# Kernel optimization log

Measured on AMD Instinct MI355X. Metric: run time of the kernel, lower is better.

Reference implementation:

```python
import jax, jax.numpy as jnp
import numpy as np

B, T, D, H, J = 64, 128, 768, 256, 128  # batch, tokens, input_dim, span_hidden_dim, top_injection_dim
PRUNING_RATIO = 2.0


def setup_inputs() -> dict:
    key = jax.random.key(0)
    ks = jax.random.split(key, 12)
    def w(k, shape, fan_in):
        return jax.random.normal(k, shape, jnp.float32) / np.sqrt(fan_in)
    return {
        "inputs": jax.random.normal(ks[0], (B, T, D), jnp.float32),
        "input_mask": jnp.ones((B, T), jnp.int32),
        "top_injection_embedding": jax.random.normal(ks[1], (B, J), jnp.float32),
        # SpanRepAssembly: start / end projections
        "W_start": w(ks[2], (D, H), D), "b_start": jnp.zeros((H,), jnp.float32),
        "W_end": w(ks[3], (D, H), D), "b_end": jnp.zeros((H,), jnp.float32),
        # span_scorer: ReLU -> Linear(H,H) -> ReLU -> Linear(H,1)
        "W_s1": w(ks[4], (H, H), H), "b_s1": jnp.zeros((H,), jnp.float32),
        "W_s2": w(ks[5], (H, 1), H), "b_s2": jnp.zeros((1,), jnp.float32),
        # top injection path
        "W_inj": w(ks[6], (J, H), J), "b_inj": jnp.zeros((H,), jnp.float32),
        "W_sec": w(ks[7], (H, H), H), "b_sec": jnp.zeros((H,), jnp.float32),
        "W_pred": w(ks[8], (H, 1), H), "b_pred": jnp.zeros((1,), jnp.float32),
    }


def reference(inputs, input_mask, top_injection_embedding,
              W_start, b_start, W_end, b_end,
              W_s1, b_s1, W_s2, b_s2,
              W_inj, b_inj, W_sec, b_sec, W_pred, b_pred):
    b, t, _ = inputs.shape
    k_spans = int(PRUNING_RATIO * t)
    # SpanRepAssembly: span_hidden[b, (s,e)] = startProj(x_s) + endProj(x_e), s <= e,
    # flattened start-major (matches start_end_range ordering).
    A = inputs @ W_start + b_start                      # [B,T,H]
    E = inputs @ W_end + b_end                          # [B,T,H]
    s_idx, e_idx = jnp.triu_indices(t)                  # N = T(T+1)/2 spans, row-major
    span_hidden = A[:, s_idx] + E[:, e_idx]             # [B,N,H]
    m = input_mask.astype(jnp.float32)
    span_mask = m[:, s_idx] * m[:, e_idx]               # [B,N]
    # span_scorer MLP over all spans
    h = jax.nn.relu(span_hidden) @ W_s1 + b_s1
    scores = (jax.nn.relu(h) @ W_s2 + b_s2)[..., 0]     # [B,N]
    # SpanPruner: mask invalid spans to -inf, top-k, sort indices, gather
    masked_scores = jnp.where(span_mask > 0, scores, -jnp.inf)
    _, top_idx = jax.lax.top_k(masked_scores, k_spans)  # [B,K]
    top_idx = jnp.sort(top_idx, axis=1)
    top_span_hidden = jnp.take_along_axis(span_hidden, top_idx[:, :, None], axis=1)  # [B,K,H]
    top_span_mask = jnp.take_along_axis(span_mask, top_idx, axis=1)[..., None]       # [B,K,1]
    top_span_scores = jnp.take_along_axis(masked_scores, top_idx, axis=1)[..., None] # [B,K,1]
    top_span_scores = jnp.where(jnp.isinf(top_span_scores), -1.0, top_span_scores)
    # top-injection scoring head
    inj = (top_injection_embedding @ W_inj + b_inj)[:, None, :]      # [B,1,H]
    sec = top_span_hidden @ W_sec + b_sec                            # [B,K,H]
    top_span_logits = jax.nn.relu(inj + sec) @ W_pred + b_pred + top_span_scores  # [B,K,1]
    top_span_probs = jax.nn.sigmoid(top_span_logits) * top_span_mask
    return top_span_probs
```

## Files before the change

kernel.cpp:

```cpp
#include <hip/hip_runtime.h>
#include <hip/hip_bf16.h>
#include <math.h>

#define BB 64
#define T 128
#define DD 768
#define H 256
#define JJ 128
#define NSPAN 8256
#define KTOP 256
#define SCAP 1024
#define MARGIN 0.03f

typedef __attribute__((ext_vector_type(8))) short bf16x8;
typedef __attribute__((ext_vector_type(4))) float f32x4;

__device__ inline unsigned short bfrne(float x) {
    unsigned u = __float_as_uint(x);
    return (unsigned short)((u + 0x7FFFu + ((u >> 16) & 1u)) >> 16);
}

__device__ inline unsigned pk2(float x, float y) {
    float2 f; f.x = x; f.y = y;
    __hip_bfloat162 h = __float22bfloat162_rn(f);
    return *reinterpret_cast<unsigned*>(&h);
}

template<int CTRL>
__device__ __forceinline__ float dpp_add16(float v) {
    return v + __int_as_float(__builtin_amdgcn_update_dpp(
        0, __float_as_int(v), CTRL, 0xF, 0xF, true));
}

__global__ __launch_bounds__(256) void prep_proj_kernel(
    const float* __restrict__ X,
    const float* __restrict__ Wa, const float* __restrict__ ba,
    const float* __restrict__ Wb, const float* __restrict__ bb,
    float* __restrict__ AE,
    int* __restrict__ s_idx, int* __restrict__ e_idx,
    const float* __restrict__ W1, unsigned short* __restrict__ Wpk,
    const float* __restrict__ tie, const float* __restrict__ Winj,
    const float* __restrict__ binj, float* __restrict__ injv)
{
    const int blk = blockIdx.x;
    const int t = threadIdx.x;

    if (blk >= 512) {
        const int pblk = blk - 512;
        if (pblk == 0) {
            if (t < T) {
                int s = t;
                int start = s * T - (s * (s - 1)) / 2;
                int len = T - s;
                for (int i = 0; i < len; ++i) {
                    s_idx[start + i] = s;
                    e_idx[start + i] = s + i;
                }
            }
        } else if (pblk <= 256) {
            int idx = (pblk - 1) * 256 + t;
            int j  = idx & 7;
            int l  = (idx >> 3) & 63;
            int kc = (idx >> 9) & 7;
            int ct = idx >> 12;
            int k = kc * 32 + (l >> 4) * 8 + j;
            int n = ct * 16 + (l & 15);
            Wpk[idx] = bfrne(W1[k * 256 + n]);
        } else {
            int b = pblk - 257;
            __shared__ float tb[JJ];
            if (t < JJ) tb[t] = tie[b * JJ + t];
            __syncthreads();
            float a = binj[t];
            for (int j = 0; j < JJ; ++j)
                a = fmaf(tb[j], Winj[j * H + t], a);
            injv[b * H + t] = a;
        }
        return;
    }

    const int px = blk & 127;
    const int cb = blk >> 7;
    const int m0 = px * 64;
    const float* W    = (cb < 2) ? Wa : Wb;
    const float* bias = (cb < 2) ? ba : bb;
    const int wc0 = (cb & 1) * 128;
    const int oc0 = (cb < 2) ? wc0 : (256 + wc0);

    __shared__ float Xs[64 * 36];
    __shared__ float Wl[32 * 132];

    const int tx = t & 15;
    const int ty = t >> 4;

    const int xrow = t >> 2;
    const int xk8  = (t & 3) * 8;
    const int wrow = t >> 4;
    const int wcol = (t & 15) * 8;

    float4 xr[2], w0r[2], w1r[2];
    {
        const float* xp = &X[(size_t)(m0 + xrow) * DD + xk8];
        xr[0] = *(const float4*)&xp[0]; xr[1] = *(const float4*)&xp[4];
        const float* wp0 = &W[(size_t)wrow * 256 + wc0 + wcol];
        w0r[0] = *(const float4*)&wp0[0]; w0r[1] = *(const float4*)&wp0[4];
        const float* wp1 = &W[(size_t)(wrow + 16) * 256 + wc0 + wcol];
        w1r[0] = *(const float4*)&wp1[0]; w1r[1] = *(const float4*)&wp1[4];
    }

    float acc[4][8];
#pragma unroll
    for (int i = 0; i < 4; ++i)
#pragma unroll
        for (int j = 0; j < 8; ++j) acc[i][j] = 0.f;

    for (int it = 0; it < 24; ++it) {
        __syncthreads();
        *(float4*)&Xs[xrow * 36 + xk8]           = xr[0];
        *(float4*)&Xs[xrow * 36 + xk8 + 4]       = xr[1];
        *(float4*)&Wl[wrow * 132 + wcol]         = w0r[0];
        *(float4*)&Wl[wrow * 132 + wcol + 4]     = w0r[1];
        *(float4*)&Wl[(wrow+16) * 132 + wcol]    = w1r[0];
        *(float4*)&Wl[(wrow+16) * 132 + wcol + 4]= w1r[1];
        __syncthreads();
        if (it + 1 < 24) {
            const int kk = (it + 1) * 32;
            const float* xp = &X[(size_t)(m0 + xrow) * DD + kk + xk8];
            xr[0] = *(const float4*)&xp[0]; xr[1] = *(const float4*)&xp[4];
            const float* wp0 = &W[(size_t)(kk + wrow) * 256 + wc0 + wcol];
            w0r[0] = *(const float4*)&wp0[0]; w0r[1] = *(const float4*)&wp0[4];
            const float* wp1 = &W[(size_t)(kk + wrow + 16) * 256 + wc0 + wcol];
            w1r[0] = *(const float4*)&wp1[0]; w1r[1] = *(const float4*)&wp1[4];
        }
#pragma unroll
        for (int k = 0; k < 32; ++k) {
            float4 wv0 = *(const float4*)&Wl[k * 132 + tx * 8];
            float4 wv1 = *(const float4*)&Wl[k * 132 + tx * 8 + 4];
            float wq[8] = {wv0.x, wv0.y, wv0.z, wv0.w, wv1.x, wv1.y, wv1.z, wv1.w};
            float xq[4];
#pragma unroll
            for (int i = 0; i < 4; ++i)
                xq[i] = Xs[(ty * 4 + i) * 36 + k];
#pragma unroll
            for (int i = 0; i < 4; ++i)
#pragma unroll
                for (int j = 0; j < 8; ++j)
                    acc[i][j] = fmaf(xq[i], wq[j], acc[i][j]);
        }
    }

    float bq[8];
#pragma unroll
    for (int j = 0; j < 8; ++j) bq[j] = bias[wc0 + tx * 8 + j];
#pragma unroll
    for (int i = 0; i < 4; ++i) {
        const size_t row = m0 + ty * 4 + i;
        float4 o0, o1;
        o0.x = acc[i][0] + bq[0]; o0.y = acc[i][1] + bq[1];
        o0.z = acc[i][2] + bq[2]; o0.w = acc[i][3] + bq[3];
        o1.x = acc[i][4] + bq[4]; o1.y = acc[i][5] + bq[5];
        o1.z = acc[i][6] + bq[6]; o1.w = acc[i][7] + bq[7];
        *(float4*)&AE[row * 512 + oc0 + tx * 8]     = o0;
        *(float4*)&AE[row * 512 + oc0 + tx * 8 + 4] = o1;
    }
}

__global__ __launch_bounds__(512, 4) void approx_kernel(
    const float* __restrict__ AE,
    const unsigned short* __restrict__ Wpk,
    const float* __restrict__ bs1, const float* __restrict__ Ws2,
    const float* __restrict__ bs2g,
    const int* __restrict__ s_idx, const int* __restrict__ e_idx,
    const int* __restrict__ maskp,
    float* __restrict__ scores)
{
    const int bid   = blockIdx.x;
    const int r     = bid & 7;
    const int q     = bid >> 3;
    const int g     = q >> 3;
    const int chunk = q & 7;
    const int b     = g * 8 + r;
    const int tile0 = chunk * 65;
    const int tcnt  = (516 - tile0 < 65) ? (516 - tile0) : 65;

    __shared__ __align__(16) unsigned short rshf[2][8][64][8];
    __shared__ float pslice[2][8][16];

    const int t      = threadIdx.x;
    const int w      = t >> 6;
    const int lane   = t & 63;
    const int lrow16 = lane & 15;
    const int quad   = lane >> 4;

    bf16x8 bfr[2][8];
    float b1c[2], w2c[2];
#pragma unroll
    for (int c = 0; c < 2; ++c) {
#pragma unroll
        for (int kc = 0; kc < 8; ++kc)
            bfr[c][kc] = *(const bf16x8*)&Wpk[((((2 * w + c) * 8 + kc) * 64) + lane) * 8];
        int col = (2 * w + c) * 16 + lrow16;
        b1c[c] = bs1[col];
        w2c[c] = Ws2[col];
    }
    const float bs2v = bs2g[0];

    const float* Abase = AE + (size_t)b * T * 512;
    const int sp   = t >> 5;
    const int km   = t & 31;
    const int kc_s = km >> 2;
    const int q_s  = km & 3;
    const int slot = (q_s * 16 + sp + kc_s) & 63;

    {
        int n = tile0 * 16 + sp;
        int s = s_idx[n], e = e_idx[n];
        const float* Ar = Abase + (size_t)s * 512 + km * 8;
        const float* Er = Abase + (size_t)e * 512 + 256 + km * 8;
        float4 a0 = *(const float4*)&Ar[0];
        float4 a1 = *(const float4*)&Ar[4];
        float4 e0 = *(const float4*)&Er[0];
        float4 e1 = *(const float4*)&Er[4];
        uint4 v;
        v.x = pk2(fmaxf(a0.x + e0.x, 0.f), fmaxf(a0.y + e0.y, 0.f));
        v.y = pk2(fmaxf(a0.z + e0.z, 0.f), fmaxf(a0.w + e0.w, 0.f));
        v.z = pk2(fmaxf(a1.x + e1.x, 0.f), fmaxf(a1.y + e1.y, 0.f));
        v.w = pk2(fmaxf(a1.z + e1.z, 0.f), fmaxf(a1.w + e1.w, 0.f));
        *(uint4*)&rshf[0][kc_s][slot][0] = v;
    }
    int s_nx = 0, e_nx = 0;
    if (tcnt > 1) {
        int n = (tile0 + 1) * 16 + sp;
        s_nx = s_idx[n]; e_nx = e_idx[n];
    }
    __syncthreads();

    for (int tt = 0; tt < tcnt; ++tt) {
        const int cur = tt & 1;
        float4 a0, a1, e0, e1;
        const bool pf = (tt + 1 < tcnt);
        if (pf) {
            const float* Ar = Abase + (size_t)s_nx * 512 + km * 8;
            const float* Er = Abase + (size_t)e_nx * 512 + 256 + km * 8;
            a0 = *(const float4*)&Ar[0];
            a1 = *(const float4*)&Ar[4];
            e0 = *(const float4*)&Er[0];
            e1 = *(const float4*)&Er[4];
        }
        if (tt + 2 < tcnt) {
            int n = (tile0 + tt + 2) * 16 + sp;
            s_nx = s_idx[n]; e_nx = e_idx[n];
        }
        f32x4 acc0 = {0.f, 0.f, 0.f, 0.f};
        f32x4 acc1 = {0.f, 0.f, 0.f, 0.f};
#pragma unroll
        for (int kc = 0; kc < 8; ++kc) {
            bf16x8 a = *(const bf16x8*)&rshf[cur][kc][(lane + kc) & 63][0];
            acc0 = __builtin_amdgcn_mfma_f32_16x16x32_bf16(a, bfr[0][kc], acc0, 0, 0, 0);
            acc1 = __builtin_amdgcn_mfma_f32_16x16x32_bf16(a, bfr[1][kc], acc1, 0, 0, 0);
        }
        float ps[4];
#pragma unroll
        for (int rr = 0; rr < 4; ++rr)
            ps[rr] = fmaxf(acc0[rr] + b1c[0], 0.f) * w2c[0]
                   + fmaxf(acc1[rr] + b1c[1], 0.f) * w2c[1];
#pragma unroll
        for (int rr = 0; rr < 4; ++rr) {
            float v = ps[rr];
            v = dpp_add16<0xB1>(v);
            v = dpp_add16<0x4E>(v);
            v = dpp_add16<0x141>(v);
            v = dpp_add16<0x140>(v);
            ps[rr] = v;
        }
        if (lrow16 == 0) {
            float4 v; v.x = ps[0]; v.y = ps[1]; v.z = ps[2]; v.w = ps[3];
            *(float4*)&pslice[cur][w][quad * 4] = v;
        }
        if (pf) {
            uint4 v;
            v.x = pk2(fmaxf(a0.x + e0.x, 0.f), fmaxf(a0.y + e0.y, 0.f));
            v.y = pk2(fmaxf(a0.z + e0.z, 0.f), fmaxf(a0.w + e0.w, 0.f));
            v.z = pk2(fmaxf(a1.x + e1.x, 0.f), fmaxf(a1.y + e1.y, 0.f));
            v.w = pk2(fmaxf(a1.z + e1.z, 0.f), fmaxf(a1.w + e1.w, 0.f));
            *(uint4*)&rshf[cur ^ 1][kc_s][slot][0] = v;
        }
        __syncthreads();
        if (t < 16) {
            int n = (tile0 + tt) * 16 + t;
            float sc = bs2v;
#pragma unroll
            for (int ww = 0; ww < 8; ++ww) sc += pslice[cur][ww][t];
            int s = s_idx[n], e = e_idx[n];
            bool m = (maskp[b * T + s] != 0) && (maskp[b * T + e] != 0);
            scores[(size_t)b * NSPAN + n] = m ? sc : -INFINITY;
        }
    }
}

__global__ __launch_bounds__(1024) void select_kernel(
    const float* __restrict__ scores,
    int* __restrict__ shortlist, int* __restrict__ slcnt)
{
    const int b = blockIdx.x;
    const int t = threadIdx.x;
    __shared__ unsigned su[NSPAN];
    __shared__ int hist[256];
    __shared__ unsigned s_prefix;
    __shared__ int s_remaining;
    __shared__ int wave_keep[16];

    const float* sc = scores + (size_t)b * NSPAN;
    for (int i = t; i < NSPAN; i += 1024) {
        unsigned ub = __float_as_uint(sc[i]);
        su[i] = (ub & 0x80000000u) ? ~ub : (ub | 0x80000000u);
    }
    __syncthreads();

    unsigned prefix = 0;
    int remaining = KTOP;
    for (int d = 3; d >= 0; --d) {
        if (t < 256) hist[t] = 0;
        __syncthreads();
        const int sh = d * 8;
        for (int i = t; i < NSPAN; i += 1024) {
            unsigned u = su[i];
            bool match = (d == 3) || ((u >> (sh + 8)) == (prefix >> (sh + 8)));
            if (match) atomicAdd(&hist[(u >> sh) & 255], 1);
        }
        __syncthreads();
        if (t == 0) {
            int acc = 0, v = 255;
            for (; v > 0; --v) {
                int h = hist[v];
                if (acc + h >= remaining) break;
                acc += h;
            }
            s_prefix = prefix | ((unsigned)v << sh);
            s_remaining = remaining - acc;
        }
        __syncthreads();
        prefix = s_prefix;
        remaining = s_remaining;
        __syncthreads();
    }

    unsigned ub = (prefix & 0x80000000u) ? (prefix & 0x7FFFFFFFu) : ~prefix;
    float kthf = __uint_as_float(ub);
    float tau = kthf - MARGIN;
    unsigned tb = __float_as_uint(tau);
    unsigned ktau = (tb & 0x80000000u) ? ~tb : (tb | 0x80000000u);

    const int wid = t >> 6, lane = t & 63;
    int base = 0;
    const unsigned long long ltmask = (1ull << lane) - 1ull;
    for (int c0 = 0; c0 < NSPAN; c0 += 1024) {
        int n = c0 + t;
        bool keep = (n < NSPAN) && (su[n] >= ktau);
        unsigned long long bk = __ballot(keep);
        int before = __popcll(bk & ltmask);
        if (lane == 0) wave_keep[wid] = __popcll(bk);
        __syncthreads();
        int kb = base;
        for (int wv = 0; wv < wid; ++wv) kb += wave_keep[wv];
        if (keep) {
            int pos = kb + before;
            if (pos < SCAP) shortlist[b * SCAP + pos] = n;
        }
        for (int wv = 0; wv < 16; ++wv) base += wave_keep[wv];
        __syncthreads();
    }
    if (t == 0) slcnt[b] = base < SCAP ? base : SCAP;
}

__global__ __launch_bounds__(512) void exact_kernel(
    const float* __restrict__ AE,
    const float* __restrict__ Ws1, const float* __restrict__ bs1,
    const float* __restrict__ Ws2, const float* __restrict__ bs2g,
    const int* __restrict__ s_idx, const int* __restrict__ e_idx,
    const int* __restrict__ shortlist, const int* __restrict__ slcnt,
    float* __restrict__ scores)
{
    const int b  = blockIdx.y;
    const int n0 = blockIdx.x * 64;
    const int cntb = slcnt[b];
    if (n0 >= cntb) return;

    __shared__ float rsh[64][36];
    __shared__ float Ws[32][260];
    __shared__ int   ss[64], se[64], nn[64];

    const int t = threadIdx.x;
    if (t < 64) {
        int row = n0 + t;
        int n = 0;
        if (row < cntb) n = shortlist[b * SCAP + row];
        nn[t] = (row < cntb) ? n : -1;
        ss[t] = s_idx[n]; se[t] = e_idx[n];
    }
    __syncthreads();

    const int tx = t & 31;
    const int ty = t >> 5;
    float acc[4][8];
#pragma unroll
    for (int i = 0; i < 4; ++i)
#pragma unroll
        for (int j = 0; j < 8; ++j) acc[i][j] = 0.f;

    const float* Abase = AE + (size_t)b * T * 512;

    for (int kk = 0; kk < 256; kk += 32) {
        __syncthreads();
        {
            int row = t >> 4, q4 = (t & 15) * 4;
#pragma unroll
            for (int q = 0; q < 4; ++q)
                *(float4*)&Ws[row][q4 + q * 64] =
                    *(const float4*)&Ws1[(size_t)(kk + row) * 256 + q4 + q * 64];
        }
        {
            int sp = t >> 3, k4 = (t & 7) * 4;
            const float* Ar = Abase + (size_t)ss[sp] * 512 + kk + k4;
            const float* Er = Abase + (size_t)se[sp] * 512 + 256 + kk + k4;
            float4 a = *(const float4*)Ar;
            float4 e = *(const float4*)Er;
            float4 v;
            v.x = fmaxf(a.x + e.x, 0.f); v.y = fmaxf(a.y + e.y, 0.f);
            v.z = fmaxf(a.z + e.z, 0.f); v.w = fmaxf(a.w + e.w, 0.f);
            *(float4*)&rsh[sp][k4] = v;
        }
        __syncthreads();
#pragma unroll
        for (int k4 = 0; k4 < 32; k4 += 4) {
            float w[4][8];
#pragma unroll
            for (int kq = 0; kq < 4; ++kq) {
                float4 w0 = *(const float4*)&Ws[k4 + kq][tx * 4];
                float4 w1 = *(const float4*)&Ws[k4 + kq][128 + tx * 4];
                w[kq][0] = w0.x; w[kq][1] = w0.y; w[kq][2] = w0.z; w[kq][3] = w0.w;
                w[kq][4] = w1.x; w[kq][5] = w1.y; w[kq][6] = w1.z; w[kq][7] = w1.w;
            }
#pragma unroll
            for (int i = 0; i < 4; ++i) {
                float4 rv = *(const float4*)&rsh[ty * 4 + i][k4];
                float rq[4] = {rv.x, rv.y, rv.z, rv.w};
#pragma unroll
                for (int kq = 0; kq < 4; ++kq)
#pragma unroll
                    for (int j = 0; j < 8; ++j)
                        acc[i][j] = fmaf(rq[kq], w[kq][j], acc[i][j]);
            }
        }
    }

    float b1[8], w2[8];
#pragma unroll
    for (int j = 0; j < 8; ++j) {
        int c = (j < 4) ? (tx * 4 + j) : (128 + tx * 4 + j - 4);
        b1[j] = bs1[c];
        w2[j] = Ws2[c];
    }
    const float bs2v = bs2g[0];
#pragma unroll
    for (int i = 0; i < 4; ++i) {
        int r = ty * 4 + i;
        float p = 0.f;
#pragma unroll
        for (int j = 0; j < 8; ++j)
            p += fmaxf(acc[i][j] + b1[j], 0.f) * w2[j];
#pragma unroll
        for (int off = 16; off > 0; off >>= 1)
            p += __shfl_down(p, off, 32);
        if (tx == 0) {
            int n = nn[r];
            if (n >= 0)
                scores[(size_t)b * NSPAN + n] = p + bs2v;
        }
    }
}

__global__ __launch_bounds__(1024) void topk_kernel(
    const float* __restrict__ scores,
    const int* __restrict__ shortlist, const int* __restrict__ slcnt,
    int* __restrict__ top_idx, float* __restrict__ top_scores)
{
    const int b = blockIdx.x;
    const int t = threadIdx.x;
    const int cnt = slcnt[b];

    __shared__ unsigned su[SCAP];
    __shared__ int sn[SCAP];
    __shared__ int hist[256];
    __shared__ unsigned s_prefix;
    __shared__ int s_remaining;
    __shared__ int wave_eq[16], wave_keep[16];

    for (int i = t; i < cnt; i += 1024) {
        int n = shortlist[b * SCAP + i];
        unsigned ub = __float_as_uint(scores[(size_t)b * NSPAN + n]);
        su[i] = (ub & 0x80000000u) ? ~ub : (ub | 0x80000000u);
        sn[i] = n;
    }
    __syncthreads();

    unsigned prefix = 0;
    int remaining = KTOP;
    for (int d = 3; d >= 0; --d) {
        if (t < 256) hist[t] = 0;
        __syncthreads();
        const int sh = d * 8;
        for (int i = t; i < cnt; i += 1024) {
            unsigned u = su[i];
            bool match = (d == 3) || ((u >> (sh + 8)) == (prefix >> (sh + 8)));
            if (match) atomicAdd(&hist[(u >> sh) & 255], 1);
        }
        __syncthreads();
        if (t == 0) {
            int acc = 0, v = 255;
            for (; v > 0; --v) {
                int h = hist[v];
                if (acc + h >= remaining) break;
                acc += h;
            }
            s_prefix = prefix | ((unsigned)v << sh);
            s_remaining = remaining - acc;
        }
        __syncthreads();
        prefix = s_prefix;
        remaining = s_remaining;
        __syncthreads();
    }
    const unsigned v = prefix;
    const int need_eq = remaining;

    const int wid = t >> 6, lane = t & 63;
    int base_eq = 0, base_keep = 0;
    const unsigned long long ltmask = (1ull << lane) - 1ull;
    for (int c0 = 0; c0 < cnt; c0 += 1024) {
        int i = c0 + t;
        bool valid = i < cnt;
        unsigned u = valid ? su[i] : 0u;
        bool eq = valid && (u == v);
        bool gt = valid && (u > v);
        unsigned long long beq = __ballot(eq);
        int eq_before = __popcll(beq & ltmask);
        if (lane == 0) wave_eq[wid] = __popcll(beq);
        __syncthreads();
        int eqb = base_eq;
        for (int w = 0; w < wid; ++w) eqb += wave_eq[w];
        int eq_rank = eqb + eq_before;
        bool keep = gt || (eq && (eq_rank < need_eq));
        unsigned long long bk = __ballot(keep);
        int keep_before = __popcll(bk & ltmask);
        if (lane == 0) wave_keep[wid] = __popcll(bk);
        __syncthreads();
        int kb = base_keep;
        for (int w = 0; w < wid; ++w) kb += wave_keep[w];
        if (keep) {
            int pos = kb + keep_before;
            top_idx[b * KTOP + pos] = sn[i];
            unsigned fb = (u & 0x80000000u) ? (u & 0x7FFFFFFFu) : ~u;
            float f = __uint_as_float(fb);
            top_scores[b * KTOP + pos] = isinf(f) ? -1.0f : f;
        }
        for (int w = 0; w < 16; ++w) { base_eq += wave_eq[w]; base_keep += wave_keep[w]; }
        __syncthreads();
    }
}

__global__ __launch_bounds__(256) void final_kernel(
    const float* __restrict__ AE,
    const int* __restrict__ s_idx, const int* __restrict__ e_idx,
    const int* __restrict__ maskp,
    const int* __restrict__ top_idx, const float* __restrict__ top_scores,
    const float* __restrict__ injv,
    const float* __restrict__ Wsec, const float* __restrict__ bsec,
    const float* __restrict__ Wpred, const float* __restrict__ bpredg,
    float* __restrict__ out)
{
    const int b = blockIdx.x >> 2;
    const int k0 = (blockIdx.x & 3) * 64;

    __shared__ float sh[64][36];
    __shared__ float Ws[32][260];
    __shared__ int ss[64], se[64];
    __shared__ float msk[64], tsc[64];

    const int t = threadIdx.x;
    if (t < 64) {
        int kidx = k0 + t;
        int n = top_idx[b * KTOP + kidx];
        int s = s_idx[n], e = e_idx[n];
        ss[t] = s; se[t] = e;
        msk[t] = (maskp[b * T + s] != 0 && maskp[b * T + e] != 0) ? 1.f : 0.f;
        tsc[t] = top_scores[b * KTOP + kidx];
    }
    __syncthreads();

    const int tx = t & 31;
    const int ty = t >> 5;
    float acc[8][8];
#pragma unroll
    for (int i = 0; i < 8; ++i)
#pragma unroll
        for (int j = 0; j < 8; ++j) acc[i][j] = 0.f;

    const float* Abase = AE + (size_t)b * T * 512;

    for (int kk = 0; kk < 256; kk += 32) {
        __syncthreads();
        {
            int c4 = (t & 63) * 4, r0 = t >> 6;
#pragma unroll
            for (int r8 = 0; r8 < 8; ++r8) {
                int row = r0 + r8 * 4;
                *(float4*)&Ws[row][c4] =
                    *(const float4*)&Wsec[(size_t)(kk + row) * 256 + c4];
            }
        }
        {
            int sp = t >> 2, k8 = (t & 3) * 8;
            const float* Ar = Abase + (size_t)ss[sp] * 512 + kk + k8;
            const float* Er = Abase + (size_t)se[sp] * 512 + 256 + kk + k8;
#pragma unroll
            for (int q = 0; q < 2; ++q) {
                float4 a = *(const float4*)&Ar[q * 4];
                float4 e = *(const float4*)&Er[q * 4];
                float4 v;
                v.x = a.x + e.x; v.y = a.y + e.y; v.z = a.z + e.z; v.w = a.w + e.w;
                *(float4*)&sh[sp][k8 + q * 4] = v;
            }
        }
        __syncthreads();
#pragma unroll
        for (int k4 = 0; k4 < 32; k4 += 4) {
            float w[4][8];
#pragma unroll
            for (int kq = 0; kq < 4; ++kq) {
                float4 w0 = *(const float4*)&Ws[k4 + kq][tx * 4];
                float4 w1 = *(const float4*)&Ws[k4 + kq][128 + tx * 4];
                w[kq][0] = w0.x; w[kq][1] = w0.y; w[kq][2] = w0.z; w[kq][3] = w0.w;
                w[kq][4] = w1.x; w[kq][5] = w1.y; w[kq][6] = w1.z; w[kq][7] = w1.w;
            }
#pragma unroll
            for (int i = 0; i < 8; ++i) {
                float4 rv = *(const float4*)&sh[ty * 8 + i][k4];
                float rq[4] = {rv.x, rv.y, rv.z, rv.w};
#pragma unroll
                for (int kq = 0; kq < 4; ++kq)
#pragma unroll
                    for (int j = 0; j < 8; ++j)
                        acc[i][j] = fmaf(rq[kq], w[kq][j], acc[i][j]);
            }
        }
    }

    float bsec_r[8], wpred_r[8], injr[8];
#pragma unroll
    for (int j = 0; j < 8; ++j) {
        int c = (j < 4) ? (tx * 4 + j) : (128 + tx * 4 + j - 4);
        bsec_r[j] = bsec[c];
        wpred_r[j] = Wpred[c];
        injr[j] = injv[b * H + c];
    }
    const float bp = bpredg[0];
#pragma unroll
    for (int i = 0; i < 8; ++i) {
        int r = ty * 8 + i;
        float p = 0.f;
#pragma unroll
        for (int j = 0; j < 8; ++j) {
            float sec = acc[i][j] + bsec_r[j];
            p += fmaxf(injr[j] + sec, 0.f) * wpred_r[j];
        }
#pragma unroll
        for (int off = 16; off > 0; off >>= 1)
            p += __shfl_down(p, off, 32);
        if (tx == 0) {
            float logit = p + bp + tsc[r];
            float prob = (1.f / (1.f + expf(-logit))) * msk[r];
            out[b * KTOP + k0 + r] = prob;
        }
    }
}

extern "C" void kernel_launch(void* const* d_in, const int* in_sizes, int n_in,
                              void* d_out, int out_size, void* d_ws, size_t ws_size,
                              hipStream_t stream) {
    const float* inputs  = (const float*)d_in[0];
    const int*   imask   = (const int*)d_in[1];
    const float* tie     = (const float*)d_in[2];
    const float* W_start = (const float*)d_in[3];
    const float* b_start = (const float*)d_in[4];
    const float* W_end   = (const float*)d_in[5];
    const float* b_end   = (const float*)d_in[6];
    const float* W_s1    = (const float*)d_in[7];
    const float* b_s1    = (const float*)d_in[8];
    const float* W_s2    = (const float*)d_in[9];
    const float* b_s2    = (const float*)d_in[10];
    const float* W_inj   = (const float*)d_in[11];
    const float* b_inj   = (const float*)d_in[12];
    const float* W_sec   = (const float*)d_in[13];
    const float* b_sec   = (const float*)d_in[14];
    const float* W_pred  = (const float*)d_in[15];
    const float* b_pred  = (const float*)d_in[16];
    float* out = (float*)d_out;

    float* AE         = (float*)d_ws;
    float* scores     = AE + (size_t)BB * T * 512;
    int*   s_idx      = (int*)(scores + (size_t)BB * NSPAN);
    int*   e_idx      = s_idx + NSPAN;
    int*   top_idx    = e_idx + NSPAN;
    float* top_scores = (float*)(top_idx + BB * KTOP);
    float* injv       = top_scores + BB * KTOP;
    unsigned short* Wpk = (unsigned short*)(injv + BB * H);
    int*   shortlist  = (int*)(Wpk + 65536);
    int*   slcnt      = shortlist + BB * SCAP;

    prep_proj_kernel<<<833, 256, 0, stream>>>(inputs, W_start, b_start, W_end, b_end, AE,
                                              s_idx, e_idx, W_s1, Wpk,
                                              tie, W_inj, b_inj, injv);
    approx_kernel<<<512, 512, 0, stream>>>(AE, Wpk, b_s1, W_s2, b_s2,
                                           s_idx, e_idx, imask, scores);
    select_kernel<<<BB, 1024, 0, stream>>>(scores, shortlist, slcnt);
    exact_kernel<<<dim3(16, BB), 512, 0, stream>>>(AE, W_s1, b_s1, W_s2, b_s2,
                                                   s_idx, e_idx, shortlist, slcnt, scores);
    topk_kernel<<<BB, 1024, 0, stream>>>(scores, shortlist, slcnt, top_idx, top_scores);
    final_kernel<<<BB * 4, 256, 0, stream>>>(AE, s_idx, e_idx, imask, top_idx, top_scores,
                                             injv, W_sec, b_sec, W_pred, b_pred, out);
}
```

Before: 484.7 us.

## Restructure projection GEMM into row-strip tiles with register-held X and double-buffered W

Rewrites the start/end projection GEMM so that each block computes 16 rows against all 512 output columns, covering Wa and Wb together. X rows are held in registers and loaded straight from global memory, while W k-tiles are double-buffered in shared memory. This replaces the earlier 64x128 tile scheme that staged both X and W through LDS. The aim is to read X from global memory only once and to cut LDS traffic and barriers per FMA. The new blocking uses many registers (xC/xN plus acc), which may limit occupancy despite the launch bound of 2. The new layout assumes the first 512 blocks cover 8192 rows at 16 rows per block, which is consistent with the existing grid.

After: 1.025 ms. 112% more time.

```diff
diff --git a/kernel.cpp b/kernel.cpp
--- a/kernel.cpp
+++ b/kernel.cpp
@@ -32,7 +32,7 @@
         0, __float_as_int(v), CTRL, 0xF, 0xF, true));
 }
 
-__global__ __launch_bounds__(256) void prep_proj_kernel(
+__global__ __launch_bounds__(256, 2) void prep_proj_kernel(
     const float* __restrict__ X,
     const float* __restrict__ Wa, const float* __restrict__ ba,
     const float* __restrict__ Wb, const float* __restrict__ bb,
@@ -79,89 +79,96 @@
         return;
     }
 
-    const int px = blk & 127;
-    const int cb = blk >> 7;
-    const int m0 = px * 64;
-    const float* W    = (cb < 2) ? Wa : Wb;
-    const float* bias = (cb < 2) ? ba : bb;
-    const int wc0 = (cb & 1) * 128;
-    const int oc0 = (cb < 2) ? wc0 : (256 + wc0);
-
-    __shared__ float Xs[64 * 36];
-    __shared__ float Wl[32 * 132];
-
-    const int tx = t & 15;
-    const int ty = t >> 4;
-
-    const int xrow = t >> 2;
-    const int xk8  = (t & 3) * 8;
-    const int wrow = t >> 4;
-    const int wcol = (t & 15) * 8;
-
-    float4 xr[2], w0r[2], w1r[2];
-    {
-        const float* xp = &X[(size_t)(m0 + xrow) * DD + xk8];
-        xr[0] = *(const float4*)&xp[0]; xr[1] = *(const float4*)&xp[4];
-        const float* wp0 = &W[(size_t)wrow * 256 + wc0 + wcol];
-        w0r[0] = *(const float4*)&wp0[0]; w0r[1] = *(const float4*)&wp0[4];
-        const float* wp1 = &W[(size_t)(wrow + 16) * 256 + wc0 + wcol];
-        w1r[0] = *(const float4*)&wp1[0]; w1r[1] = *(const float4*)&wp1[4];
-    }
-
-    float acc[4][8];
-#pragma unroll
-    for (int i = 0; i < 4; ++i)
-#pragma unroll
-        for (int j = 0; j < 8; ++j) acc[i][j] = 0.f;
-
-    for (int it = 0; it < 24; ++it) {
-        __syncthreads();
-        *(float4*)&Xs[xrow * 36 + xk8]           = xr[0];
-        *(float4*)&Xs[xrow * 36 + xk8 + 4]       = xr[1];
-        *(float4*)&Wl[wrow * 132 + wcol]         = w0r[0];
-        *(float4*)&Wl[wrow * 132 + wcol + 4]     = w0r[1];
-        *(float4*)&Wl[(wrow+16) * 132 + wcol]    = w1r[0];
-        *(float4*)&Wl[(wrow+16) * 132 + wcol + 4]= w1r[1];
-        __syncthreads();
-        if (it + 1 < 24) {
-            const int kk = (it + 1) * 32;
-            const float* xp = &X[(size_t)(m0 + xrow) * DD + kk + xk8];
-            xr[0] = *(const float4*)&xp[0]; xr[1] = *(const float4*)&xp[4];
-            const float* wp0 = &W[(size_t)(kk + wrow) * 256 + wc0 + wcol];
-            w0r[0] = *(const float4*)&wp0[0]; w0r[1] = *(const float4*)&wp0[4];
-            const float* wp1 = &W[(size_t)(kk + wrow + 16) * 256 + wc0 + wcol];
-            w1r[0] = *(const float4*)&wp1[0]; w1r[1] = *(const float4*)&wp1[4];
-        }
-#pragma unroll
-        for (int k = 0; k < 32; ++k) {
-            float4 wv0 = *(const float4*)&Wl[k * 132 + tx * 8];
-            float4 wv1 = *(const float4*)&Wl[k * 132 + tx * 8 + 4];
-            float wq[8] = {wv0.x, wv0.y, wv0.z, wv0.w, wv1.x, wv1.y, wv1.z, wv1.w};
-            float xq[4];
-#pragma unroll
-            for (int i = 0; i < 4; ++i)
-                xq[i] = Xs[(ty * 4 + i) * 36 + k];
-#pragma unroll
-            for (int i = 0; i < 4; ++i)
-#pragma unroll
-                for (int j = 0; j < 8; ++j)
-                    acc[i][j] = fmaf(xq[i], wq[j], acc[i][j]);
-        }
-    }
-
-    float bq[8];
-#pragma unroll
-    for (int j = 0; j < 8; ++j) bq[j] = bias[wc0 + tx * 8 + j];
-#pragma unroll
-    for (int i = 0; i < 4; ++i) {
-        const size_t row = m0 + ty * 4 + i;
-        float4 o0, o1;
-        o0.x = acc[i][0] + bq[0]; o0.y = acc[i][1] + bq[1];
-        o0.z = acc[i][2] + bq[2]; o0.w = acc[i][3] + bq[3];
-        o1.x = acc[i][4] + bq[4]; o1.y = acc[i][5] + bq[5];
-        o1.z = acc[i][6] + bq[6]; o1.w = acc[i][7] + bq[7];
-        *(float4*)&AE[row * 512 + oc0 + tx * 8]     = o0;
-        *(float4*)&AE[row * 512 + oc0 + tx * 8 + 4] = o1;
+    const int m0   = blk * 16;
+    const int w    = t >> 6;
+    const int lane = t & 63;
+    const int rg   = w >> 1;
+    const int hf   = w & 1;
+    const int r0   = m0 + rg * 8;
+    const int cl   = lane * 4;
+
+    __shared__ __align__(16) float Wt[2][8][512];
+
+    float4 wreg[4];
+    float4 xC[16], xN[16];
+    float4 acc[8];
+
+    auto stageW_load = [&](int tileIdx) {
+#pragma unroll
+        for (int i = 0; i < 4; ++i) {
+            const int j  = w * 4 + i;
+            const int kr = j >> 1, jh = j & 1;
+            const float* src = (jh ? Wb : Wa) + (size_t)(tileIdx * 8 + kr) * 256 + cl;
+            wreg[i] = *(const float4*)src;
+        }
+    };
+    auto stageW_write = [&](float (*dst)[512]) {
+#pragma unroll
+        for (int i = 0; i < 4; ++i) {
+            const int j  = w * 4 + i;
+            const int kr = j >> 1, jh = j & 1;
+            *(float4*)&dst[kr][jh * 256 + cl] = wreg[i];
+        }
+    };
+    auto loadX = [&](float4 (&xr)[16], int tileIdx) {
+        const int kk = tileIdx * 8;
+#pragma unroll
+        for (int r = 0; r < 8; ++r) {
+            const float* xp = &X[(size_t)(r0 + r) * DD + kk];
+            xr[r * 2]     = *(const float4*)&xp[0];
+            xr[r * 2 + 1] = *(const float4*)&xp[4];
+        }
+    };
+    auto compute8 = [&](const float4 (&xr)[16], const float* wb) {
+#pragma unroll
+        for (int kq = 0; kq < 8; ++kq) {
+            const float4 wv = *(const float4*)(wb + kq * 512);
+#pragma unroll
+            for (int r = 0; r < 8; ++r) {
+                const float4 xv4 = xr[r * 2 + (kq >> 2)];
+                const float xv = (kq & 3) == 0 ? xv4.x
+                               : (kq & 3) == 1 ? xv4.y
+                               : (kq & 3) == 2 ? xv4.z : xv4.w;
+                acc[r].x = fmaf(xv, wv.x, acc[r].x);
+                acc[r].y = fmaf(xv, wv.y, acc[r].y);
+                acc[r].z = fmaf(xv, wv.z, acc[r].z);
+                acc[r].w = fmaf(xv, wv.w, acc[r].w);
+            }
+        }
+    };
+
+    const float* w0 = &Wt[0][0][hf * 256 + cl];
+    const float* w1 = &Wt[1][0][hf * 256 + cl];
+
+#pragma unroll
+    for (int r = 0; r < 8; ++r) { acc[r].x = 0.f; acc[r].y = 0.f; acc[r].z = 0.f; acc[r].w = 0.f; }
+
+    stageW_load(0);
+    loadX(xC, 0);
+    stageW_write(Wt[0]);
+    __syncthreads();
+
+    for (int tile = 0; tile < 96; tile += 2) {
+        stageW_load(tile + 1);
+        loadX(xN, tile + 1);
+        compute8(xC, w0);
+        stageW_write(Wt[1]);
+        __syncthreads();
+        const bool more = (tile + 2) < 96;
+        if (more) { stageW_load(tile + 2); loadX(xC, tile + 2); }
+        compute8(xN, w1);
+        if (more) stageW_write(Wt[0]);
+        __syncthreads();
+    }
+
+    const float* bsel = hf ? bb : ba;
+    const float4 bq = *(const float4*)&bsel[cl];
+#pragma unroll
+    for (int r = 0; r < 8; ++r) {
+        float4 o;
+        o.x = acc[r].x + bq.x; o.y = acc[r].y + bq.y;
+        o.z = acc[r].z + bq.z; o.w = acc[r].w + bq.w;
+        *(float4*)&AE[(size_t)(r0 + r) * 512 + hf * 256 + cl] = o;
     }
 }
 
```
